# Kernel optimization log

Hardware: AMD Instinct MI355X
Metric: run time of the kernel (lower is better)

## Reference

```python
import jax, jax.numpy as jnp
import numpy as np

IMAGE = 128            # canvas_size == image_size -> resize is identity
N_LINES = 32
N_SEGMENTS = 2
N_POINTS = 5           # control points per line (2 shared-endpoint quadratic beziers)
N_COLOR = 3
COORDPAIRS = np.array([[0, 1, 2], [2, 3, 4]])  # (n_segments, 3)
N_SAMPLES = 10         # polyline samples for bezier edt2 (explicit 10 in source)
POWER = 2.0            # power at progress=0 (= config.power_i)
SIGMA2 = 0.05          # annealed sigma2 at progress=0
EPS = 1e-10
BS = 4


def setup_inputs() -> dict:
    key = jax.random.key(0)
    k1, k2, k3, k4 = jax.random.split(key, 4)
    position = 0.5 * jax.random.normal(k1, (BS, N_LINES, N_POINTS * 2), jnp.float32)
    radius = jax.random.uniform(k2, (BS, N_LINES, 1), jnp.float32, minval=0.3, maxval=1.0)
    color = jax.random.uniform(k3, (BS, N_LINES, N_COLOR), jnp.float32)
    background = jax.random.uniform(k4, (BS, N_COLOR), jnp.float32)
    return {"position": position, "radius": radius, "color": color, "background": background}


def _render(position, radius, color, background):
    bs = position.shape[0]
    r = jnp.linspace(-1.0, 1.0, IMAGE)
    gy, gx = jnp.meshgrid(r, r, indexing="ij")
    grid = jnp.stack([gy, gx], axis=-1)                      # (H, W, 2)

    # --- reshape_params (background='keep', n_back=0) ---
    lines = position.reshape(bs, N_LINES, N_POINTS, 2)
    segs = lines[:, :, COORDPAIRS]                           # (bs, nl, nseg, 3, 2)
    # smooth bezier: reflect control point of segments after the first
    segs = segs.at[:, :, 1:, 1].set(2.0 * segs[:, :, 1:, 0] - segs[:, :, 1:, 1])
    curves = segs.reshape(bs, N_LINES * N_SEGMENTS, 3, 2)    # (bs, N, 3, 2)

    sigma = (radius ** 2).reshape(bs, N_LINES, 1, 1)
    sigma = jnp.repeat(sigma, N_SEGMENTS, axis=1) * SIGMA2   # (bs, N, 1, 1)
    col = jnp.repeat(color, N_SEGMENTS, axis=1)[:, :, :, None, None]  # (bs, N, nc, 1, 1)

    # --- curve_edt2_polyline: sample quadratic bezier, min segment distance ---
    t = jnp.linspace(0.0, 1.0, N_SAMPLES)
    w = jnp.stack([(1.0 - t) ** 2, 2.0 * t * (1.0 - t), t ** 2], axis=0)  # (3, T)
    pts = jnp.einsum("bnkc,kt->bntc", curves, w)             # (bs, N, T, 2)
    a, b = pts[:, :, :-1], pts[:, :, 1:]                     # (bs, N, S=T-1, 2)
    v = b - a
    v_ = v[:, :, :, None, None, :]
    d = grid[None, None, None] - a[:, :, :, None, None, :]   # (bs, N, S, H, W, 2)
    vv = jnp.sum(v * v, axis=-1)[:, :, :, None, None]
    tp = jnp.clip(jnp.sum(d * v_, axis=-1) / (vv + EPS), 0.0, 1.0)
    diff = d - tp[..., None] * v_
    edt2 = jnp.min(jnp.sum(diff * diff, axis=-1), axis=2)    # (bs, N, H, W)

    # --- intensity + rasterize + over-composite ---
    intensity = jnp.exp(-((edt2 / sigma) ** POWER))          # (bs, N, H, W)
    rasters = col * intensity[:, :, None]                    # (bs, N, nc, H, W)
    canvas = jnp.broadcast_to(background[:, None, :, None, None],
                              (bs, 1, N_COLOR, IMAGE, IMAGE))
    rasters = jnp.concatenate([rasters, canvas], axis=1)     # (bs, N+1, nc, H, W)
    inten_c = jnp.broadcast_to(intensity[:, :, None],
                               (bs, intensity.shape[1], N_COLOR, IMAGE, IMAGE))
    inten_all = jnp.concatenate([inten_c, jnp.ones_like(canvas)], axis=1)
    linv = 1.0 - inten_all + EPS
    # 'over' composite front-to-back along stroke dim: exclusive cumprod weights
    w_excl = jnp.concatenate([jnp.ones_like(linv[:, :1]),
                              jnp.cumprod(linv, axis=1)[:, :-1]], axis=1)
    images = jnp.sum(rasters * w_excl, axis=1)               # (bs, nc, H, W)
    return jnp.clip(images, 0.0, 1.0)


def reference(position, radius, color, background):
    return _render(position, radius, color, background)
```

## Files before the change

### kernel.cpp

```cpp
#include <hip/hip_runtime.h>

#define IMAGE   128
#define NLINES  32
#define NCURVE  64
#define NSUB    9
#define PIX     (IMAGE*IMAGE)
#define BS      4
#define NCHUNK  8
#define CPC     8

#define RECF 64

__global__ __launch_bounds__(256)
void setup_kernel(const float* __restrict__ pos,
                  const float* __restrict__ rad,
                  const float* __restrict__ col,
                  float* __restrict__ tbl)
{
    const int tid = threadIdx.x;
    for (int e = tid; e < BS*NCURVE*NSUB; e += 256) {
        const int j = e % NSUB;
        const int n = (e / NSUB) & (NCURVE-1);
        const int b = e / (NSUB*NCURVE);
        const int line = n >> 1;
        const int seg  = n & 1;
        const float* P = pos + (b*NLINES + line)*10;
        float c0x, c0y, c1x, c1y, c2x, c2y;
        if (seg == 0) {
            c0x = P[0]; c0y = P[1];
            c1x = P[2]; c1y = P[3];
            c2x = P[4]; c2y = P[5];
        } else {
            const float q2x = P[4], q2y = P[5];
            const float q3x = P[6], q3y = P[7];
            c0x = q2x;             c0y = q2y;
            c1x = 2.0f*q2x - q3x;  c1y = 2.0f*q2y - q3y;
            c2x = P[8];            c2y = P[9];
        }
        const float t0 = (float)j     * (1.0f/9.0f);
        const float t1 = (float)(j+1) * (1.0f/9.0f);
        float ax, ay, bx, by;
        {
            const float mt = 1.0f - t0;
            const float w0 = mt*mt, w1 = 2.0f*t0*mt, w2 = t0*t0;
            ax = w0*c0x + w1*c1x + w2*c2x;
            ay = w0*c0y + w1*c1y + w2*c2y;
        }
        {
            const float mt = 1.0f - t1;
            const float w0 = mt*mt, w1 = 2.0f*t1*mt, w2 = t1*t1;
            bx = w0*c0x + w1*c1x + w2*c2x;
            by = w0*c0y + w1*c1y + w2*c2y;
        }
        const float vx = bx - ax, vy = by - ay;
        float* base = tbl + (b*NCURVE + n)*RECF;
        base[j*4+0] = ax; base[j*4+1] = ay;
        base[j*4+2] = vx; base[j*4+3] = vy;
        base[36+j]  = 1.0f / (vx*vx + vy*vy + 1e-10f);
    }
    {
        const int b = tid >> 6, n = tid & (NCURVE-1);
        const int line = n >> 1;
        const float r = rad[b*NLINES + line];
        float* base = tbl + tid*RECF;
        base[48] = 1.0f / (r*r*0.05f);
        base[49] = col[(b*NLINES + line)*3 + 0];
        base[50] = col[(b*NLINES + line)*3 + 1];
        base[51] = col[(b*NLINES + line)*3 + 2];
    }
}

__global__ __launch_bounds__(512, 8)
void render_kernel(const float* __restrict__ tbl,
                   const float* __restrict__ bg,
                   float* __restrict__ out)
{
    __shared__ float4 s_part[NCHUNK*64];

    const int tid   = threadIdx.x;
    const int b     = blockIdx.x >> 8;
    const int tile  = blockIdx.x & 255;
    const int px    = tid & 63;
    const int chunk = __builtin_amdgcn_readfirstlane(tid >> 6);

    const int p = tile*64 + px;
    const float g0 = -1.0f + (float)(p >> 7)  * (2.0f/127.0f);
    const float g1 = -1.0f + (float)(p & 127) * (2.0f/127.0f);

    float aR = 0.0f, aG = 0.0f, aB = 0.0f, T = 1.0f;
    for (int i = 0; i < CPC; ++i) {
        const int n = chunk*CPC + i;
        const float* __restrict__ base = tbl + (b*NCURVE + n)*RECF;
        float edt2 = 3.4e38f;
        #pragma unroll
        for (int j = 0; j < NSUB; ++j) {
            const float ax = base[j*4+0], ay = base[j*4+1];
            const float vx = base[j*4+2], vy = base[j*4+3];
            const float rvv = base[36+j];
            const float d0  = g0 - ax;
            const float d1  = g1 - ay;
            const float dt  = d0*vx + d1*vy;
            const float tp  = fminf(fmaxf(dt*rvv, 0.0f), 1.0f);
            const float e0  = d0 - tp*vx;
            const float e1  = d1 - tp*vy;
            edt2 = fminf(edt2, e0*e0 + e1*e1);
        }
        const float xs = edt2 * base[48];
        const float I  = __expf(-xs*xs);
        const float wI = I * T;
        aR = fmaf(base[49], wI, aR);
        aG = fmaf(base[50], wI, aG);
        aB = fmaf(base[51], wI, aB);
        T *= (1.0f - I + 1e-10f);
    }
    s_part[chunk*64 + px] = make_float4(aR, aG, aB, T);
    __syncthreads();

    if (tid < 64) {
        float4 acc = s_part[tid];
        float C0 = acc.x, C1 = acc.y, C2 = acc.z, Tt = acc.w;
        #pragma unroll
        for (int c = 1; c < NCHUNK; ++c) {
            const float4 q = s_part[c*64 + tid];
            C0 = fmaf(Tt, q.x, C0);
            C1 = fmaf(Tt, q.y, C1);
            C2 = fmaf(Tt, q.z, C2);
            Tt *= q.w;
        }
        C0 = fmaf(Tt, bg[b*3+0], C0);
        C1 = fmaf(Tt, bg[b*3+1], C1);
        C2 = fmaf(Tt, bg[b*3+2], C2);
        const int po = tile*64 + tid;
        out[(b*3+0)*PIX + po] = fminf(fmaxf(C0, 0.0f), 1.0f);
        out[(b*3+1)*PIX + po] = fminf(fmaxf(C1, 0.0f), 1.0f);
        out[(b*3+2)*PIX + po] = fminf(fmaxf(C2, 0.0f), 1.0f);
    }
}

extern "C" void kernel_launch(void* const* d_in, const int* in_sizes, int n_in,
                              void* d_out, int out_size, void* d_ws, size_t ws_size,
                              hipStream_t stream) {
    const float* pos = (const float*)d_in[0];
    const float* rad = (const float*)d_in[1];
    const float* col = (const float*)d_in[2];
    const float* bg  = (const float*)d_in[3];
    float* out = (float*)d_out;
    float* tbl = (float*)d_ws;

    setup_kernel<<<dim3(1), dim3(256), 0, stream>>>(pos, rad, col, tbl);
    render_kernel<<<dim3(BS*256), dim3(512), 0, stream>>>(tbl, bg, out);
}
```

Baseline: 74.12 us.

## Fuse setup into render kernel, building per-batch segment table in LDS

Removes the separate single-block setup kernel. Each render block now recomputes the segment table for its own batch and keeps it in shared memory, replacing scalar global loads from the workspace table with LDS loads. The distance math is reworked to precompute v/|v|^2 and use FMAs. The inner loop unroll drops to 3. This saves a kernel launch and its serial dependency, but every block now repeats the setup work and pays LDS traffic plus a sync, and it loses the uniform scalar loads the old version used.

```diff
diff --git a/kernel.cpp b/kernel.cpp
--- a/kernel.cpp
+++ b/kernel.cpp
@@ -9,19 +9,25 @@
 #define NCHUNK  8
 #define CPC     8
 
-#define RECF 64
+__global__ __launch_bounds__(512, 8)
+void render_kernel(const float* __restrict__ pos,
+                   const float* __restrict__ rad,
+                   const float* __restrict__ col,
+                   const float* __restrict__ bg,
+                   float* __restrict__ out)
+{
+    __shared__ float4 s_sub4[NCURVE*NSUB];
+    __shared__ float2 s_sub2[NCURVE*NSUB];
+    __shared__ float4 s_cur[NCURVE];
+    __shared__ float4 s_part[NCHUNK*64];
 
-__global__ __launch_bounds__(256)
-void setup_kernel(const float* __restrict__ pos,
-                  const float* __restrict__ rad,
-                  const float* __restrict__ col,
-                  float* __restrict__ tbl)
-{
-    const int tid = threadIdx.x;
-    for (int e = tid; e < BS*NCURVE*NSUB; e += 256) {
-        const int j = e % NSUB;
-        const int n = (e / NSUB) & (NCURVE-1);
-        const int b = e / (NSUB*NCURVE);
+    const int tid  = threadIdx.x;
+    const int b    = blockIdx.x >> 8;
+    const int tile = blockIdx.x & 255;
+
+    for (int e = tid; e < NCURVE*NSUB; e += 512) {
+        const int n    = e / NSUB;
+        const int j    = e - n*NSUB;
         const int line = n >> 1;
         const int seg  = n & 1;
         const float* P = pos + (b*NLINES + line)*10;
@@ -53,64 +59,48 @@
             by = w0*c0y + w1*c1y + w2*c2y;
         }
         const float vx = bx - ax, vy = by - ay;
-        float* base = tbl + (b*NCURVE + n)*RECF;
-        base[j*4+0] = ax; base[j*4+1] = ay;
-        base[j*4+2] = vx; base[j*4+3] = vy;
-        base[36+j]  = 1.0f / (vx*vx + vy*vy + 1e-10f);
+        const float rvv = 1.0f / (vx*vx + vy*vy + 1e-10f);
+        s_sub4[e] = make_float4(ax, ay, vx, vy);
+        s_sub2[e] = make_float2(vx*rvv, vy*rvv);
     }
-    {
-        const int b = tid >> 6, n = tid & (NCURVE-1);
-        const int line = n >> 1;
-        const float r = rad[b*NLINES + line];
-        float* base = tbl + tid*RECF;
-        base[48] = 1.0f / (r*r*0.05f);
-        base[49] = col[(b*NLINES + line)*3 + 0];
-        base[50] = col[(b*NLINES + line)*3 + 1];
-        base[51] = col[(b*NLINES + line)*3 + 2];
+    if (tid < NCURVE) {
+        const int line = tid >> 1;
+        const float r  = rad[b*NLINES + line];
+        s_cur[tid] = make_float4(1.0f / (r*r*0.05f),
+                                 col[(b*NLINES + line)*3 + 0],
+                                 col[(b*NLINES + line)*3 + 1],
+                                 col[(b*NLINES + line)*3 + 2]);
     }
-}
+    __syncthreads();
 
-__global__ __launch_bounds__(512, 8)
-void render_kernel(const float* __restrict__ tbl,
-                   const float* __restrict__ bg,
-                   float* __restrict__ out)
-{
-    __shared__ float4 s_part[NCHUNK*64];
-
-    const int tid   = threadIdx.x;
-    const int b     = blockIdx.x >> 8;
-    const int tile  = blockIdx.x & 255;
     const int px    = tid & 63;
-    const int chunk = __builtin_amdgcn_readfirstlane(tid >> 6);
-
-    const int p = tile*64 + px;
-    const float g0 = -1.0f + (float)(p >> 7)  * (2.0f/127.0f);
-    const float g1 = -1.0f + (float)(p & 127) * (2.0f/127.0f);
+    const int chunk = tid >> 6;
+    const int p     = tile*64 + px;
+    const float g0  = -1.0f + (float)(p >> 7)  * (2.0f/127.0f);
+    const float g1  = -1.0f + (float)(p & 127) * (2.0f/127.0f);
 
     float aR = 0.0f, aG = 0.0f, aB = 0.0f, T = 1.0f;
     for (int i = 0; i < CPC; ++i) {
         const int n = chunk*CPC + i;
-        const float* __restrict__ base = tbl + (b*NCURVE + n)*RECF;
         float edt2 = 3.4e38f;
-        #pragma unroll
+        #pragma unroll 3
         for (int j = 0; j < NSUB; ++j) {
-            const float ax = base[j*4+0], ay = base[j*4+1];
-            const float vx = base[j*4+2], vy = base[j*4+3];
-            const float rvv = base[36+j];
-            const float d0  = g0 - ax;
-            const float d1  = g1 - ay;
-            const float dt  = d0*vx + d1*vy;
-            const float tp  = fminf(fmaxf(dt*rvv, 0.0f), 1.0f);
-            const float e0  = d0 - tp*vx;
-            const float e1  = d1 - tp*vy;
-            edt2 = fminf(edt2, e0*e0 + e1*e1);
+            const float4 s = s_sub4[n*NSUB + j];
+            const float2 w = s_sub2[n*NSUB + j];
+            const float d0 = g0 - s.x;
+            const float d1 = g1 - s.y;
+            const float tp = fminf(fmaxf(d0*w.x + d1*w.y, 0.0f), 1.0f);
+            const float e0 = fmaf(-tp, s.z, d0);
+            const float e1 = fmaf(-tp, s.w, d1);
+            edt2 = fminf(edt2, fmaf(e0, e0, e1*e1));
         }
-        const float xs = edt2 * base[48];
-        const float I  = __expf(-xs*xs);
-        const float wI = I * T;
-        aR = fmaf(base[49], wI, aR);
-        aG = fmaf(base[50], wI, aG);
-        aB = fmaf(base[51], wI, aB);
+        const float4 cu = s_cur[n];
+        const float xs  = edt2 * cu.x;
+        const float I   = __expf(-xs*xs);
+        const float wI  = I * T;
+        aR = fmaf(cu.y, wI, aR);
+        aG = fmaf(cu.z, wI, aG);
+        aB = fmaf(cu.w, wI, aB);
         T *= (1.0f - I + 1e-10f);
     }
     s_part[chunk*64 + px] = make_float4(aR, aG, aB, T);
@@ -145,8 +135,6 @@
     const float* col = (const float*)d_in[2];
     const float* bg  = (const float*)d_in[3];
     float* out = (float*)d_out;
-    float* tbl = (float*)d_ws;
 
-    setup_kernel<<<dim3(1), dim3(256), 0, stream>>>(pos, rad, col, tbl);
-    render_kernel<<<dim3(BS*256), dim3(512), 0, stream>>>(tbl, bg, out);
+    render_kernel<<<dim3(BS*256), dim3(512), 0, stream>>>(pos, rad, col, bg, out);
 }
```

Result: faster. 70.08 us (-5.5%).
